# Optimization experiments

Hardware: AMD Instinct MI355X
Metric: run time of the kernel (lower is better)

Reference implementation:

```python
import jax, jax.numpy as jnp
import numpy as np

D_MODEL = 1024
NUM_HEADS = 16
D_HEAD = D_MODEL // NUM_HEADS
BATCH, SEQ, MEM = 2, 1024, 1024
TOT = SEQ + MEM


def setup_inputs() -> dict:
    key = jax.random.key(0)
    ks = jax.random.split(key, 16)
    s = 0.02
    return {
        "x": jax.random.normal(ks[0], (BATCH, SEQ, D_MODEL), jnp.float32),
        "mem": jax.random.normal(ks[1], (BATCH, MEM, D_MODEL), jnp.float32),
        "mask": jnp.zeros((1, 1, SEQ, TOT), jnp.float32),
        "rel_enc": jax.random.normal(ks[2], (TOT, D_MODEL), jnp.float32),
        "Wq": jax.random.normal(ks[3], (D_MODEL, D_MODEL), jnp.float32) * s,
        "bq": jnp.zeros((D_MODEL,), jnp.float32),
        "Wke": jax.random.normal(ks[4], (D_MODEL, D_MODEL), jnp.float32) * s,
        "bke": jnp.zeros((D_MODEL,), jnp.float32),
        "Wkr": jax.random.normal(ks[5], (D_MODEL, D_MODEL), jnp.float32) * s,
        "bkr": jnp.zeros((D_MODEL,), jnp.float32),
        "Wv": jax.random.normal(ks[6], (D_MODEL, D_MODEL), jnp.float32) * s,
        "bv": jnp.zeros((D_MODEL,), jnp.float32),
        "Wo": jax.random.normal(ks[7], (D_MODEL, D_MODEL), jnp.float32) * s,
        "bo": jnp.zeros((D_MODEL,), jnp.float32),
    }


def _split_heads(t, b):
    # (b, s, d_model) -> (b, h, s, d_head)
    return t.reshape(b, -1, NUM_HEADS, D_HEAD).transpose(0, 2, 1, 3)


def _rel_enc_shift(arr):
    # arr: (b, h, l, m) -> Transformer-XL shift trick
    b, h, l, m = arr.shape
    arr = jnp.concatenate([arr, jnp.zeros((b, h, l, 1), arr.dtype)], axis=-1)
    arr = arr.reshape(b, h, l * (m + 1))
    return arr[:, :, l - 1:-1].reshape(b, h, l, m)


def reference(x, mem, mask, rel_enc, Wq, bq, Wke, bke, Wkr, bkr, Wv, bv, Wo, bo):
    b, s, _ = x.shape
    x_tilde = jnp.concatenate([mem, x], axis=1)  # (b, tot, d)
    q = _split_heads(x @ Wq + bq, b)             # (b, h, s, dh)
    k = _split_heads(x_tilde @ Wke + bke, b)     # (b, h, tot, dh)
    v = _split_heads(x_tilde @ Wv + bv, b)       # (b, h, tot, dh)
    A = jnp.einsum("bhsd,bhtd->bhst", q, k)      # content scores
    Q = (rel_enc @ Wkr + bkr).reshape(-1, NUM_HEADS, D_HEAD).transpose(1, 0, 2)  # (h, tot, dh)
    B_hat = jnp.einsum("bhsd,htd->bhst", q, Q)
    B = _rel_enc_shift(B_hat)                    # relative-position scores
    scores = (A + B) / jnp.sqrt(jnp.float32(D_HEAD)) + mask * -1e9
    w = jax.nn.softmax(scores, axis=-1)
    out = jnp.einsum("bhst,bhtd->bhsd", w, v)
    out = out.transpose(0, 2, 1, 3).reshape(b, s, D_MODEL)
    return out @ Wo + bo
```

## Files before the change

### kernel.cpp

```cpp
#include <hip/hip_runtime.h>

typedef unsigned short ushort;
typedef unsigned int uint;
typedef __attribute__((ext_vector_type(8))) short short8;
typedef __attribute__((ext_vector_type(4))) float float4v;

#define D_MODEL 1024
#define NH 16
#define DH 64
#define BATCH 2
#define SEQ 1024
#define MEMLEN 1024
#define TOT 2048

__device__ __forceinline__ float b2f(ushort u) {
  return __uint_as_float(((uint)u) << 16);
}
__device__ __forceinline__ ushort f2b(float f) {
  uint i = __float_as_uint(f);
  uint r = (i + 0x7fffu + ((i >> 16) & 1u)) >> 16;
  return (ushort)r;
}
__device__ __forceinline__ void gld16(const ushort* g, ushort* l) {
  __builtin_amdgcn_global_load_lds(
      (const __attribute__((address_space(1))) void*)g,
      (__attribute__((address_space(3))) void*)l, 16, 0, 0);
}

__global__ __launch_bounds__(256) void preproc_kernel(
    const float* __restrict__ x, const float* __restrict__ mem,
    const float* __restrict__ rel, const float* __restrict__ mask,
    ushort* __restrict__ xt, ushort* __restrict__ xb,
    ushort* __restrict__ relb, ushort* __restrict__ maskb) {
  const int bid = blockIdx.x;
  if (bid < 2048) {
    int idx = bid * 256 + threadIdx.x;
    int row = idx >> 7;
    int c8 = (idx & 127) << 3;
    int b = row >> 11;
    int i = row & 2047;
    const float* src = (i < MEMLEN) ? &mem[((b << 10) + i) * D_MODEL]
                                    : &x[((b << 10) + (i - MEMLEN)) * D_MODEL];
    float4 f0 = *(const float4*)(&src[c8]);
    float4 f1 = *(const float4*)(&src[c8 + 4]);
    ushort u[8] = {f2b(f0.x), f2b(f0.y), f2b(f0.z), f2b(f0.w),
                   f2b(f1.x), f2b(f1.y), f2b(f1.z), f2b(f1.w)};
    *(uint4*)(&xt[row * D_MODEL + c8]) = *(const uint4*)u;
    if (i >= MEMLEN)
      *(uint4*)(&xb[((b << 10) + (i - MEMLEN)) * D_MODEL + c8]) =
          *(const uint4*)u;
  } else if (bid < 3072) {
    int idx = (bid - 2048) * 256 + threadIdx.x;
    int base = idx << 3;
    float4 f0 = *(const float4*)(&rel[base]);
    float4 f1 = *(const float4*)(&rel[base + 4]);
    ushort u[8] = {f2b(f0.x), f2b(f0.y), f2b(f0.z), f2b(f0.w),
                   f2b(f1.x), f2b(f1.y), f2b(f1.z), f2b(f1.w)};
    *(uint4*)(&relb[base]) = *(const uint4*)u;
  } else {
    int idx = (bid - 3072) * 256 + threadIdx.x;
    int base = idx << 3;
    float4 f0 = *(const float4*)(&mask[base]);
    float4 f1 = *(const float4*)(&mask[base + 4]);
    ushort u[8] = {f2b(f0.x * -1e9f), f2b(f0.y * -1e9f), f2b(f0.z * -1e9f),
                   f2b(f0.w * -1e9f), f2b(f1.x * -1e9f), f2b(f1.y * -1e9f),
                   f2b(f1.z * -1e9f), f2b(f1.w * -1e9f)};
    *(uint4*)(&maskb[base]) = *(const uint4*)u;
  }
}

__global__ __launch_bounds__(256) void transpose_cvt5_kernel(
    const float* __restrict__ W0, const float* __restrict__ W1,
    const float* __restrict__ W2, const float* __restrict__ W3,
    const float* __restrict__ W4, ushort* __restrict__ T0,
    ushort* __restrict__ T1, ushort* __restrict__ T2, ushort* __restrict__ T3,
    ushort* __restrict__ T4) {
  __shared__ ushort tle[32][33];
  const float* W;
  ushort* T;
  switch (blockIdx.z) {
    case 0: W = W0; T = T0; break;
    case 1: W = W1; T = T1; break;
    case 2: W = W2; T = T2; break;
    case 3: W = W3; T = T3; break;
    default: W = W4; T = T4; break;
  }
  const int bx = blockIdx.x * 32, by = blockIdx.y * 32;
  const int tx = threadIdx.x & 31, ty = threadIdx.x >> 5;
#pragma unroll
  for (int j = 0; j < 32; j += 8)
    tle[ty + j][tx] = f2b(W[(by + ty + j) * 1024 + bx + tx]);
  __syncthreads();
#pragma unroll
  for (int j = 0; j < 32; j += 8)
    T[(bx + ty + j) * 1024 + by + tx] = tle[tx][ty + j];
}

__global__ __launch_bounds__(256) void gemm_fused_kernel(
    const ushort* __restrict__ xt, const ushort* __restrict__ xbrel,
    const ushort* __restrict__ WkeT, const ushort* __restrict__ WqT,
    const ushort* __restrict__ WkrT, const float* __restrict__ bke,
    const float* __restrict__ bv, const float* __restrict__ bq,
    const float* __restrict__ bkr, ushort* __restrict__ kv,
    ushort* __restrict__ qr) {
  __shared__ ushort As[128 * 32];
  __shared__ ushort Bs[128 * 32];
  const int bid = blockIdx.x;
  const bool seg0 = (bid < 512);
  const ushort* A;
  const ushort* BT;
  int m0, n0;
  if (seg0) {
    m0 = (bid & 31) * 128;
    n0 = (bid >> 5) * 128;
    A = xt;
    BT = WkeT;
  } else {
    int g = bid - 512;
    m0 = (g & 31) * 128;
    n0 = (g >> 5) * 128;
    A = xbrel;
    BT = (m0 < 2048) ? WqT : WkrT;
  }
  const int tid = threadIdx.x;
  const int w = tid >> 6, lane = tid & 63, m15 = lane & 15, q4 = lane >> 4;
  const int wm = w & 1, wn = w >> 1;
  float4v acc[4][4] = {};
  const int c0 = tid, c1 = tid + 256;
  const int r0 = c0 >> 2, u0 = (c0 & 3) * 8;
  const int r1 = c1 >> 2, u1 = (c1 & 3) * 8;

  for (int kk = 0; kk < 1024; kk += 32) {
    __syncthreads();
    gld16(&A[(m0 + r0) * 1024 + kk + u0], &As[c0 * 8]);
    gld16(&A[(m0 + r1) * 1024 + kk + u1], &As[c1 * 8]);
    gld16(&BT[(n0 + r0) * 1024 + kk + u0], &Bs[c0 * 8]);
    gld16(&BT[(n0 + r1) * 1024 + kk + u1], &Bs[c1 * 8]);
    __syncthreads();
    short8 af[4], bf[4];
#pragma unroll
    for (int i = 0; i < 4; ++i)
      af[i] = *(const short8*)(&As[(wm * 64 + i * 16 + m15) * 32 + q4 * 8]);
#pragma unroll
    for (int j = 0; j < 4; ++j)
      bf[j] = *(const short8*)(&Bs[(wn * 64 + j * 16 + m15) * 32 + q4 * 8]);
#pragma unroll
    for (int i = 0; i < 4; ++i)
#pragma unroll
      for (int j = 0; j < 4; ++j)
        acc[i][j] =
            __builtin_amdgcn_mfma_f32_16x16x32_bf16(af[i], bf[j], acc[i][j], 0, 0, 0);
  }
#pragma unroll
  for (int j = 0; j < 4; ++j) {
    int col = n0 + wn * 64 + j * 16 + m15;
    if (seg0) {
      if (col < 1024) {
        float bb = bke[col];
#pragma unroll
        for (int i = 0; i < 4; ++i) {
          int rowb = m0 + wm * 64 + i * 16 + q4 * 4;
#pragma unroll
          for (int r = 0; r < 4; ++r)
            kv[(rowb + r) * 2048 + col] = f2b((acc[i][j][r] + bb) * 0.125f);
        }
      } else {
        float bb = bv[col - 1024];
#pragma unroll
        for (int i = 0; i < 4; ++i) {
          int rowb = m0 + wm * 64 + i * 16 + q4 * 4;
          int dg = ((rowb >> 11) << 10) + (col - 1024);
          size_t prow = (size_t)(dg * 2 + ((rowb >> 10) & 1)) * 2048 + 1024 +
                        (rowb & 1023);
          uint lo = (uint)f2b(acc[i][j][0] + bb) |
                    ((uint)f2b(acc[i][j][1] + bb) << 16);
          uint hi = (uint)f2b(acc[i][j][2] + bb) |
                    ((uint)f2b(acc[i][j][3] + bb) << 16);
          *(uint2*)(&kv[prow]) = make_uint2(lo, hi);
        }
      }
    } else {
      float bb = (m0 < 2048) ? bq[col] : bkr[col];
      float sc = (m0 < 2048) ? 1.0f : 0.125f;
#pragma unroll
      for (int i = 0; i < 4; ++i) {
        int rowb = m0 + wm * 64 + i * 16 + q4 * 4;
#pragma unroll
        for (int r = 0; r < 4; ++r)
          qr[(rowb + r) * 1024 + col] = f2b((acc[i][j][r] + bb) * sc);
      }
    }
  }
}

template <int EPI>
__global__ __launch_bounds__(256) void gemm64_kernel(
    const ushort* __restrict__ A, const ushort* __restrict__ BT,
    const float* __restrict__ bias, void* __restrict__ Cout, int M, int N,
    int K) {
  __shared__ ushort As[64 * 32];
  __shared__ ushort Bs[128 * 32];
  const int m0 = blockIdx.x * 64, n0 = blockIdx.y * 128;
  const int tid = threadIdx.x;
  const int w = tid >> 6, lane = tid & 63, m15 = lane & 15, q4 = lane >> 4;
  float4v acc[4][2] = {};
  const int ra = tid >> 2, ua = (tid & 3) * 8;
  const int c0 = tid, c1 = tid + 256;
  const int rb0 = c0 >> 2, ub0 = (c0 & 3) * 8;
  const int rb1 = c1 >> 2, ub1 = (c1 & 3) * 8;

  for (int kk = 0; kk < K; kk += 32) {
    __syncthreads();
    gld16(&A[(m0 + ra) * K + kk + ua], &As[tid * 8]);
    gld16(&BT[(n0 + rb0) * K + kk + ub0], &Bs[c0 * 8]);
    gld16(&BT[(n0 + rb1) * K + kk + ub1], &Bs[c1 * 8]);
    __syncthreads();
    short8 bf[2];
#pragma unroll
    for (int j = 0; j < 2; ++j)
      bf[j] = *(const short8*)(&Bs[(w * 32 + j * 16 + m15) * 32 + q4 * 8]);
#pragma unroll
    for (int i = 0; i < 4; ++i) {
      short8 af = *(const short8*)(&As[(i * 16 + m15) * 32 + q4 * 8]);
#pragma unroll
      for (int j = 0; j < 2; ++j)
        acc[i][j] =
            __builtin_amdgcn_mfma_f32_16x16x32_bf16(af, bf[j], acc[i][j], 0, 0, 0);
    }
  }
#pragma unroll
  for (int j = 0; j < 2; ++j) {
    int col = n0 + w * 32 + j * 16 + m15;
    float bv = bias[col];
#pragma unroll
    for (int i = 0; i < 4; ++i) {
      int rowb = m0 + i * 16 + q4 * 4;
#pragma unroll
      for (int r = 0; r < 4; ++r) {
        float v = acc[i][j][r] + bv;
        if (EPI == 1)
          ((float*)Cout)[(rowb + r) * N + col] = v;
        else
          ((ushort*)Cout)[(rowb + r) * N + col] = f2b(v);
      }
    }
  }
}

__global__ __launch_bounds__(256) void bhat_kernel(
    const ushort* __restrict__ q, const ushort* __restrict__ Qrb,
    const ushort* __restrict__ maskb, ushort* __restrict__ Bh) {
  __shared__ ushort As[2 * 128 * 32];
  __shared__ ushort Bs[2 * 128 * 32];
  const int bs0 = blockIdx.x * 128, u0 = blockIdx.y * 128, h = blockIdx.z;
  const int tid = threadIdx.x;
  const int w = tid >> 6, lane = tid & 63, m15 = lane & 15, q4 = lane >> 4;
  const int wm = w & 1, wn = w >> 1;

#pragma unroll
  for (int c = 0; c < 4; ++c) {
    int unit = c * 256 + tid;
    int row = (unit >> 2) & 127, kh = unit >> 9, cu = unit & 3;
    gld16(&q[(bs0 + row) * 1024 + (h << 6) + kh * 32 + cu * 8], &As[unit * 8]);
    gld16(&Qrb[(u0 + row) * 1024 + (h << 6) + kh * 32 + cu * 8], &Bs[unit * 8]);
  }
  __syncthreads();

  float4v acc[4][4] = {};
#pragma unroll
  for (int kh = 0; kh < 2; ++kh) {
    short8 af[4], bf[4];
#pragma unroll
    for (int i = 0; i < 4; ++i)
      af[i] = *(const short8*)(&As[kh * 4096 + (wm * 64 + i * 16 + m15) * 32 + q4 * 8]);
#pragma unroll
    for (int j = 0; j < 4; ++j)
      bf[j] = *(const short8*)(&Bs[kh * 4096 + (wn * 64 + j * 16 + m15) * 32 + q4 * 8]);
#pragma unroll
    for (int i = 0; i < 4; ++i)
#pragma unroll
      for (int j = 0; j < 4; ++j)
        acc[i][j] =
            __builtin_amdgcn_mfma_f32_16x16x32_bf16(af[i], bf[j], acc[i][j], 0, 0, 0);
  }
  const int b = bs0 >> 10;
  const int s0loc = bs0 & 1023;
  const int outrow0 = ((b << 4) + h) * 1024 + s0loc;
#pragma unroll
  for (int j = 0; j < 4; ++j) {
    int u = u0 + wn * 64 + j * 16 + m15;
#pragma unroll
    for (int i = 0; i < 4; ++i) {
      int rowb = outrow0 + wm * 64 + i * 16 + q4 * 4;
      int spb = s0loc + wm * 64 + i * 16 + q4 * 4;
#pragma unroll
      for (int r = 0; r < 4; ++r) {
        int sp = spb + r;
        bool selA = (u >= 1023 - sp);
        int mrow = selA ? sp : (sp > 0 ? sp - 1 : 0);
        int mcol = selA ? (u + sp - 1023) : (u + sp + 1025);
        float mval = b2f(maskb[mrow * 2048 + mcol]);
        Bh[(rowb + r) * 2048 + u] = f2b(acc[i][j][r] + mval);
      }
    }
  }
}

__global__ __launch_bounds__(256, 2) void attn_kernel(
    const ushort* __restrict__ qb, const ushort* __restrict__ kv,
    const ushort* __restrict__ Bh, const ushort* __restrict__ maskb,
    ushort* __restrict__ attn) {
  __shared__ ushort Pp[4][16 * 36];
  __shared__ float comb[2][16][68];
  __shared__ float csum[32];

  const int tid = threadIdx.x;
  const int w = tid >> 6, lane = tid & 63, m15 = lane & 15, q4 = lane >> 4;
  const int st = w & 1, th = w >> 1;
  const int s0w = blockIdx.x * 32 + st * 16;
  const int h = blockIdx.y, b = blockIdx.z;
  const int s_l = q4 * 4;

  const ushort* qp = &qb[((b << 10) + s0w + m15) * 1024 + (h << 6) + q4 * 8];
  const short8 af0 = *(const short8*)qp;
  const short8 af1 = *(const short8*)(qp + 32);

  const ushort* kvb = &kv[((size_t)(b << 11) * 2048) + (h << 6)];
  const ushort* vrowb =
      &kv[((size_t)(((b << 10) + (h << 6)) << 1) + th) * 2048 + 1024];
  const int bhbase = ((b << 4) + h) << 21;
  ushort* pw = &Pp[w][0];

  int offA[4], offB[4], diagT[4];
  float dm[4];
#pragma unroll
  for (int i = 0; i < 4; ++i) {
    int s = s0w + s_l + i;
    offA[i] = bhbase + (s << 11) - s + 1023;
    offB[i] = bhbase + ((s + 1) << 11) - s - 1026;
    diagT[i] = s + 1025;
    dm[i] = (diagT[i] <= 2047) ? b2f(maskb[s * 2048 + diagT[i]]) : 0.f;
  }

  float lsum4[4] = {0.f, 0.f, 0.f, 0.f};
  float4v oacc[4] = {};
  const int tb = th * 1024;

  auto ldKV = [&](int c, short8 (&K)[2][2], short8 (&V)[4]) {
    const int t0 = tb + c * 32;
#pragma unroll
    for (int nt = 0; nt < 2; ++nt) {
      const ushort* kp = &kvb[(size_t)(t0 + nt * 16 + m15) * 2048 + q4 * 8];
      K[nt][0] = *(const short8*)kp;
      K[nt][1] = *(const short8*)(kp + 32);
    }
    const int tc = c * 32 + q4 * 8;
#pragma unroll
    for (int nd = 0; nd < 4; ++nd)
      V[nd] = *(const short8*)(&vrowb[(size_t)(nd * 16 + m15) * 4096 + tc]);
  };
  auto ldB = [&](int c, ushort (&B)[8]) {
    const int t0 = tb + c * 32;
#pragma unroll
    for (int nt = 0; nt < 2; ++nt)
#pragma unroll
      for (int i = 0; i < 4; ++i) {
        int t = t0 + nt * 16 + m15;
        int off = (t < diagT[i]) ? offA[i] : offB[i];
        B[nt * 4 + i] = Bh[off + t];
      }
  };

  auto chunk = [&](int c, short8 (&K)[2][2], short8 (&V)[4],
                   short8 (&Kp)[2][2], short8 (&Vp)[4], ushort (&Bs)[8]) {
    ushort cur[8];
#pragma unroll
    for (int j = 0; j < 8; ++j) cur[j] = Bs[j];
    if (c + 2 < 32) ldKV(c + 2, Kp, Vp);
    __builtin_amdgcn_sched_barrier(0x38F);
    if (c + 4 < 32) ldB(c + 4, Bs);
    __builtin_amdgcn_sched_barrier(0x38F);
    float4v a0 = {}, a1 = {};
    a0 = __builtin_amdgcn_mfma_f32_16x16x32_bf16(af0, K[0][0], a0, 0, 0, 0);
    a0 = __builtin_amdgcn_mfma_f32_16x16x32_bf16(af1, K[0][1], a0, 0, 0, 0);
    a1 = __builtin_amdgcn_mfma_f32_16x16x32_bf16(af0, K[1][0], a1, 0, 0, 0);
    a1 = __builtin_amdgcn_mfma_f32_16x16x32_bf16(af1, K[1][1], a1, 0, 0, 0);
    const int t0 = tb + c * 32;
#pragma unroll
    for (int nt = 0; nt < 2; ++nt)
#pragma unroll
      for (int i = 0; i < 4; ++i) {
        int t = t0 + nt * 16 + m15;
        float bv = (t == diagT[i]) ? dm[i] : b2f(cur[nt * 4 + i]);
        float a = (nt == 0) ? a0[i] : a1[i];
        float p = __expf(a + bv);
        lsum4[i] += p;
        pw[(s_l + i) * 36 + nt * 16 + m15] = f2b(p);
      }
    short8 pfr = *(const short8*)(&pw[m15 * 36 + q4 * 8]);
#pragma unroll
    for (int nd = 0; nd < 4; ++nd)
      oacc[nd] =
          __builtin_amdgcn_mfma_f32_16x16x32_bf16(pfr, V[nd], oacc[nd], 0, 0, 0);
  };

  short8 K0[2][2], V0[4], K1[2][2], V1[4], K2[2][2], V2[4], K3[2][2], V3[4];
  ushort B0[8], B1[8], B2[8], B3[8];
  ldKV(0, K0, V0);
  ldKV(1, K1, V1);
  __builtin_amdgcn_sched_barrier(0x38F);
  ldB(0, B0);
  ldB(1, B1);
  ldB(2, B2);
  ldB(3, B3);
  __builtin_amdgcn_sched_barrier(0x38F);
  for (int j = 0; j < 8; ++j) {
    const int c = j * 4;
    chunk(c, K0, V0, K2, V2, B0);
    chunk(c + 1, K1, V1, K3, V3, B1);
    chunk(c + 2, K2, V2, K0, V0, B2);
    chunk(c + 3, K3, V3, K1, V1, B3);
  }

#pragma unroll
  for (int i = 0; i < 4; ++i) {
    float v = lsum4[i];
    v += __shfl_xor(v, 1, 64);
    v += __shfl_xor(v, 2, 64);
    v += __shfl_xor(v, 4, 64);
    v += __shfl_xor(v, 8, 64);
    lsum4[i] = v;
  }
  if (th == 1) {
#pragma unroll
    for (int nd = 0; nd < 4; ++nd)
#pragma unroll
      for (int i = 0; i < 4; ++i)
        comb[st][s_l + i][nd * 16 + m15] = oacc[nd][i];
    if (m15 == 0)
#pragma unroll
      for (int i = 0; i < 4; ++i) csum[st * 16 + s_l + i] = lsum4[i];
  }
  __syncthreads();
  if (th == 0) {
#pragma unroll
    for (int i = 0; i < 4; ++i) lsum4[i] += csum[st * 16 + s_l + i];
#pragma unroll
    for (int nd = 0; nd < 4; ++nd)
#pragma unroll
      for (int i = 0; i < 4; ++i) {
        float v = oacc[nd][i] + comb[st][s_l + i][nd * 16 + m15];
        attn[((b << 10) + s0w + s_l + i) * 1024 + (h << 6) + nd * 16 + m15] =
            f2b(v / lsum4[i]);
      }
  }
}

extern "C" void kernel_launch(void* const* d_in, const int* in_sizes, int n_in,
                              void* d_out, int out_size, void* d_ws,
                              size_t ws_size, hipStream_t stream) {
  const float* x = (const float*)d_in[0];
  const float* mem = (const float*)d_in[1];
  const float* mask = (const float*)d_in[2];
  const float* rel = (const float*)d_in[3];
  const float* Wq = (const float*)d_in[4];
  const float* bq = (const float*)d_in[5];
  const float* Wke = (const float*)d_in[6];
  const float* bke = (const float*)d_in[7];
  const float* Wkr = (const float*)d_in[8];
  const float* bkr = (const float*)d_in[9];
  const float* Wv = (const float*)d_in[10];
  const float* bv = (const float*)d_in[11];
  const float* Wo = (const float*)d_in[12];
  const float* bo = (const float*)d_in[13];
  float* out = (float*)d_out;

  ushort* ws = (ushort*)d_ws;
  ushort* xt = ws;
  ushort* xbrel = xt + 4096 * 1024;
  ushort* WqT = xbrel + 4096 * 1024;
  ushort* WkeT = WqT + 1024 * 1024;
  ushort* WvT = WkeT + 1024 * 1024;
  ushort* WkrT = WvT + 1024 * 1024;
  ushort* WoT = WkrT + 1024 * 1024;
  ushort* kv = WoT + 1024 * 1024;
  ushort* qr = kv + 4096 * 2048;
  ushort* attn = qr + 4096 * 1024;
  ushort* maskb = attn + 2048 * 1024;
  ushort* Bh = maskb + 1024 * 2048;
  ushort* relb = xbrel + 2048 * 1024;
  ushort* Qrb = qr + 2048 * 1024;

  preproc_kernel<<<4096, 256, 0, stream>>>(x, mem, rel, mask, xt, xbrel, relb,
                                           maskb);
  transpose_cvt5_kernel<<<dim3(32, 32, 5), 256, 0, stream>>>(
      Wq, Wke, Wkr, Wv, Wo, WqT, WkeT, WkrT, WvT, WoT);

  gemm_fused_kernel<<<768, 256, 0, stream>>>(xt, xbrel, WkeT, WqT, WkrT, bke,
                                             bv, bq, bkr, kv, qr);

  bhat_kernel<<<dim3(16, 16, 16), 256, 0, stream>>>(qr, Qrb, maskb, Bh);

  attn_kernel<<<dim3(SEQ / 32, NH, BATCH), 256, 0, stream>>>(qr, kv, Bh, maskb,
                                                             attn);

  gemm64_kernel<1><<<dim3(32, 8), 256, 0, stream>>>(attn, WoT, bo, out, 2048,
                                                    1024, 1024);
}
```

Measured before the change: 366.4 us.

## Stage K/V/B-hat tiles through LDS with async loads in attention kernel

The attention kernel now uses 64 query rows per block, with each wave owning 16 rows and running over all 2048 keys. This replaces the split-key scheme and its cross-wave combine step. K, V and the shifted B-hat rows are brought into swizzled LDS through a 4-slot global_load_lds pipeline, and explicit vmcnt waits and barriers replace per-thread scattered register loads. The B-hat buffer gets a padded, row-skewed layout (BROW=2056) so that the shifted reads become 16-byte aligned vectors, with a dual-buffer fallback for tiles that straddle the diagonal. In exchange the block count is halved, per-block LDS use grows, and the new indexing adds correctness risk.

```diff
diff --git a/kernel.cpp b/kernel.cpp
--- a/kernel.cpp
+++ b/kernel.cpp
@@ -12,6 +12,8 @@
 #define SEQ 1024
 #define MEMLEN 1024
 #define TOT 2048
+#define BROW 2056
+#define PLN (1024 * BROW)
 
 __device__ __forceinline__ float b2f(ushort u) {
   return __uint_as_float(((uint)u) << 16);
@@ -285,13 +287,12 @@
   }
   const int b = bs0 >> 10;
   const int s0loc = bs0 & 1023;
-  const int outrow0 = ((b << 4) + h) * 1024 + s0loc;
+  const int pbase = ((b << 4) + h) * PLN;
 #pragma unroll
   for (int j = 0; j < 4; ++j) {
     int u = u0 + wn * 64 + j * 16 + m15;
 #pragma unroll
     for (int i = 0; i < 4; ++i) {
-      int rowb = outrow0 + wm * 64 + i * 16 + q4 * 4;
       int spb = s0loc + wm * 64 + i * 16 + q4 * 4;
 #pragma unroll
       for (int r = 0; r < 4; ++r) {
@@ -300,127 +301,160 @@
         int mrow = selA ? sp : (sp > 0 ? sp - 1 : 0);
         int mcol = selA ? (u + sp - 1023) : (u + sp + 1025);
         float mval = b2f(maskb[mrow * 2048 + mcol]);
-        Bh[(rowb + r) * 2048 + u] = f2b(acc[i][j][r] + mval);
+        Bh[pbase + sp * BROW + ((sp + 1) & 7) + u] = f2b(acc[i][j][r] + mval);
       }
     }
   }
 }
 
-__global__ __launch_bounds__(256, 2) void attn_kernel(
+__global__ __launch_bounds__(256) void attn_kernel(
     const ushort* __restrict__ qb, const ushort* __restrict__ kv,
     const ushort* __restrict__ Bh, const ushort* __restrict__ maskb,
     ushort* __restrict__ attn) {
+  __shared__ ushort Ks[4][32 * 64];
+  __shared__ ushort Vs[4][64 * 32];
+  __shared__ ushort BA[4][64 * 32];
+  __shared__ ushort BB[4][64 * 32];
   __shared__ ushort Pp[4][16 * 36];
-  __shared__ float comb[2][16][68];
-  __shared__ float csum[32];
 
   const int tid = threadIdx.x;
   const int w = tid >> 6, lane = tid & 63, m15 = lane & 15, q4 = lane >> 4;
-  const int st = w & 1, th = w >> 1;
-  const int s0w = blockIdx.x * 32 + st * 16;
+  const int s0 = blockIdx.x * 64;
   const int h = blockIdx.y, b = blockIdx.z;
   const int s_l = q4 * 4;
-
-  const ushort* qp = &qb[((b << 10) + s0w + m15) * 1024 + (h << 6) + q4 * 8];
+  const int sw0 = s0 + w * 16;
+
+  const ushort* qp = &qb[((b << 10) + sw0 + m15) * 1024 + (h << 6) + q4 * 8];
   const short8 af0 = *(const short8*)qp;
   const short8 af1 = *(const short8*)(qp + 32);
 
   const ushort* kvb = &kv[((size_t)(b << 11) * 2048) + (h << 6)];
-  const ushort* vrowb =
-      &kv[((size_t)(((b << 10) + (h << 6)) << 1) + th) * 2048 + 1024];
-  const int bhbase = ((b << 4) + h) << 21;
+  const size_t vbase = ((size_t)((b << 10) + (h << 6)) * 2) * 2048;
+  const int pbase = ((b << 4) + h) * PLN;
   ushort* pw = &Pp[w][0];
 
-  int offA[4], offB[4], diagT[4];
   float dm[4];
+  int diagT[4];
 #pragma unroll
   for (int i = 0; i < 4; ++i) {
-    int s = s0w + s_l + i;
-    offA[i] = bhbase + (s << 11) - s + 1023;
-    offB[i] = bhbase + ((s + 1) << 11) - s - 1026;
+    int s = sw0 + s_l + i;
     diagT[i] = s + 1025;
     dm[i] = (diagT[i] <= 2047) ? b2f(maskb[s * 2048 + diagT[i]]) : 0.f;
   }
+  asm volatile("s_waitcnt vmcnt(0)" ::: "memory");
+  __builtin_amdgcn_sched_barrier(0);
+
+  const int rK = tid >> 3, cK = tid & 7;
+  const int rV = tid >> 2, cV = tid & 3;
+  const int rB = tid >> 2, cB = tid & 3;
+  const int sB = s0 + rB;
+  const int offA_l = pbase + sB * BROW + ((sB + 1) & 7) - sB + 1023;
+  const int offB_l = pbase + (sB + 1) * BROW + ((sB + 2) & 7) - sB - 1026;
+  const int segK = cK ^ (rK & 7);
+  const int segV = cV ^ ((rV >> 2) & 3);
+  const int segB = cB ^ ((rB >> 2) & 3);
 
   float lsum4[4] = {0.f, 0.f, 0.f, 0.f};
   float4v oacc[4] = {};
-  const int tb = th * 1024;
-
-  auto ldKV = [&](int c, short8 (&K)[2][2], short8 (&V)[4]) {
-    const int t0 = tb + c * 32;
-#pragma unroll
-    for (int nt = 0; nt < 2; ++nt) {
-      const ushort* kp = &kvb[(size_t)(t0 + nt * 16 + m15) * 2048 + q4 * 8];
-      K[nt][0] = *(const short8*)kp;
-      K[nt][1] = *(const short8*)(kp + 32);
+
+#define STAGE(c, sl)                                                          \
+  {                                                                           \
+    const int t0_ = (c) * 32;                                                 \
+    gld16(&kvb[(size_t)(t0_ + rK) * 2048 + segK * 8], &Ks[sl][tid * 8]);      \
+    gld16(&kv[vbase + ((size_t)rV * 2 + (t0_ >> 10)) * 2048 + 1024 +          \
+              (t0_ & 1023) + segV * 8],                                       \
+          &Vs[sl][tid * 8]);                                                  \
+    int t8_ = t0_ + segB * 8;                                                 \
+    int offa_ = (t8_ <= sB + 1025) ? offA_l : offB_l;                         \
+    gld16(&Bh[offa_ + t8_], &BA[sl][tid * 8]);                                \
+    bool str_ = (t0_ + 31 >= s0 + 1018) && (t0_ <= s0 + 1088);                \
+    int offb_ = str_ ? offB_l : offa_;                                        \
+    gld16(&Bh[offb_ + t8_], &BB[sl][tid * 8]);                                \
+  }
+
+#define WAITV(n)                                                              \
+  __builtin_amdgcn_sched_barrier(0);                                          \
+  asm volatile("s_waitcnt vmcnt(" #n ")" ::: "memory");                       \
+  __builtin_amdgcn_sched_barrier(0);                                          \
+  __builtin_amdgcn_s_barrier();
+
+  auto compute = [&](int c, int sl) {
+    const int t0 = c * 32;
+    short8 Kf[2][2];
+#pragma unroll
+    for (int nt = 0; nt < 2; ++nt)
+#pragma unroll
+      for (int ko = 0; ko < 2; ++ko)
+        Kf[nt][ko] = *(const short8*)(&Ks[sl][(nt * 16 + m15) * 64 +
+                                              (((q4 + 4 * ko) ^ (m15 & 7)) << 3)]);
+    short8 Vf[4];
+#pragma unroll
+    for (int nd = 0; nd < 4; ++nd) {
+      int d = nd * 16 + m15;
+      Vf[nd] = *(const short8*)(&Vs[sl][d * 32 + ((q4 ^ ((d >> 2) & 3)) << 3)]);
     }
-    const int tc = c * 32 + q4 * 8;
-#pragma unroll
-    for (int nd = 0; nd < 4; ++nd)
-      V[nd] = *(const short8*)(&vrowb[(size_t)(nd * 16 + m15) * 4096 + tc]);
-  };
-  auto ldB = [&](int c, ushort (&B)[8]) {
-    const int t0 = tb + c * 32;
-#pragma unroll
-    for (int nt = 0; nt < 2; ++nt)
-#pragma unroll
-      for (int i = 0; i < 4; ++i) {
-        int t = t0 + nt * 16 + m15;
-        int off = (t < diagT[i]) ? offA[i] : offB[i];
-        B[nt * 4 + i] = Bh[off + t];
-      }
-  };
-
-  auto chunk = [&](int c, short8 (&K)[2][2], short8 (&V)[4],
-                   short8 (&Kp)[2][2], short8 (&Vp)[4], ushort (&Bs)[8]) {
-    ushort cur[8];
-#pragma unroll
-    for (int j = 0; j < 8; ++j) cur[j] = Bs[j];
-    if (c + 2 < 32) ldKV(c + 2, Kp, Vp);
-    __builtin_amdgcn_sched_barrier(0x38F);
-    if (c + 4 < 32) ldB(c + 4, Bs);
-    __builtin_amdgcn_sched_barrier(0x38F);
     float4v a0 = {}, a1 = {};
-    a0 = __builtin_amdgcn_mfma_f32_16x16x32_bf16(af0, K[0][0], a0, 0, 0, 0);
-    a0 = __builtin_amdgcn_mfma_f32_16x16x32_bf16(af1, K[0][1], a0, 0, 0, 0);
-    a1 = __builtin_amdgcn_mfma_f32_16x16x32_bf16(af0, K[1][0], a1, 0, 0, 0);
-    a1 = __builtin_amdgcn_mfma_f32_16x16x32_bf16(af1, K[1][1], a1, 0, 0, 0);
-    const int t0 = tb + c * 32;
-#pragma unroll
-    for (int nt = 0; nt < 2; ++nt)
-#pragma unroll
-      for (int i = 0; i < 4; ++i) {
-        int t = t0 + nt * 16 + m15;
-        float bv = (t == diagT[i]) ? dm[i] : b2f(cur[nt * 4 + i]);
-        float a = (nt == 0) ? a0[i] : a1[i];
-        float p = __expf(a + bv);
-        lsum4[i] += p;
-        pw[(s_l + i) * 36 + nt * 16 + m15] = f2b(p);
-      }
+    a0 = __builtin_amdgcn_mfma_f32_16x16x32_bf16(af0, Kf[0][0], a0, 0, 0, 0);
+    a0 = __builtin_amdgcn_mfma_f32_16x16x32_bf16(af1, Kf[0][1], a0, 0, 0, 0);
+    a1 = __builtin_amdgcn_mfma_f32_16x16x32_bf16(af0, Kf[1][0], a1, 0, 0, 0);
+    a1 = __builtin_amdgcn_mfma_f32_16x16x32_bf16(af1, Kf[1][1], a1, 0, 0, 0);
+    const bool strad = (t0 + 31 >= s0 + 1018) && (t0 <= s0 + 1088);
+    if (!strad) {
+#pragma unroll
+      for (int nt = 0; nt < 2; ++nt)
+#pragma unroll
+        for (int i = 0; i < 4; ++i) {
+          int rr = (w << 4) + s_l + i;
+          int cc = nt * 16 + m15;
+          ushort bu = BA[sl][rr * 32 + (((cc >> 3) ^ q4) << 3) + (cc & 7)];
+          float a = nt ? a1[i] : a0[i];
+          float p = __expf(a + b2f(bu));
+          lsum4[i] += p;
+          pw[(s_l + i) * 36 + cc] = f2b(p);
+        }
+    } else {
+#pragma unroll
+      for (int nt = 0; nt < 2; ++nt)
+#pragma unroll
+        for (int i = 0; i < 4; ++i) {
+          int rr = (w << 4) + s_l + i;
+          int cc = nt * 16 + m15;
+          int t = t0 + cc;
+          int li = rr * 32 + (((cc >> 3) ^ q4) << 3) + (cc & 7);
+          int s = sw0 + s_l + i;
+          float va = b2f(BA[sl][li]);
+          float vb = b2f(BB[sl][li]);
+          int t8 = t & ~7;
+          float bval = (t == diagT[i])
+                           ? dm[i]
+                           : ((t > diagT[i] && t8 <= s + 1025) ? vb : va);
+          float a = nt ? a1[i] : a0[i];
+          float p = __expf(a + bval);
+          lsum4[i] += p;
+          pw[(s_l + i) * 36 + cc] = f2b(p);
+        }
+    }
     short8 pfr = *(const short8*)(&pw[m15 * 36 + q4 * 8]);
 #pragma unroll
     for (int nd = 0; nd < 4; ++nd)
       oacc[nd] =
-          __builtin_amdgcn_mfma_f32_16x16x32_bf16(pfr, V[nd], oacc[nd], 0, 0, 0);
+          __builtin_amdgcn_mfma_f32_16x16x32_bf16(pfr, Vf[nd], oacc[nd], 0, 0, 0);
   };
 
-  short8 K0[2][2], V0[4], K1[2][2], V1[4], K2[2][2], V2[4], K3[2][2], V3[4];
-  ushort B0[8], B1[8], B2[8], B3[8];
-  ldKV(0, K0, V0);
-  ldKV(1, K1, V1);
-  __builtin_amdgcn_sched_barrier(0x38F);
-  ldB(0, B0);
-  ldB(1, B1);
-  ldB(2, B2);
-  ldB(3, B3);
-  __builtin_amdgcn_sched_barrier(0x38F);
-  for (int j = 0; j < 8; ++j) {
+  STAGE(0, 0);
+  STAGE(1, 1);
+  STAGE(2, 2);
+  for (int j = 0; j < 15; ++j) {
     const int c = j * 4;
-    chunk(c, K0, V0, K2, V2, B0);
-    chunk(c + 1, K1, V1, K3, V3, B1);
-    chunk(c + 2, K2, V2, K0, V0, B2);
-    chunk(c + 3, K3, V3, K1, V1, B3);
-  }
+    STAGE(c + 3, 3); WAITV(12); compute(c, 0); __builtin_amdgcn_s_barrier();
+    STAGE(c + 4, 0); WAITV(12); compute(c + 1, 1); __builtin_amdgcn_s_barrier();
+    STAGE(c + 5, 1); WAITV(12); compute(c + 2, 2); __builtin_amdgcn_s_barrier();
+    STAGE(c + 6, 2); WAITV(12); compute(c + 3, 3); __builtin_amdgcn_s_barrier();
+  }
+  STAGE(63, 3); WAITV(12); compute(60, 0); __builtin_amdgcn_s_barrier();
+  WAITV(8);  compute(61, 1); __builtin_amdgcn_s_barrier();
+  WAITV(4);  compute(62, 2); __builtin_amdgcn_s_barrier();
+  WAITV(0);  compute(63, 3);
 
 #pragma unroll
   for (int i = 0; i < 4; ++i) {
@@ -431,29 +465,14 @@
     v += __shfl_xor(v, 8, 64);
     lsum4[i] = v;
   }
-  if (th == 1) {
-#pragma unroll
-    for (int nd = 0; nd < 4; ++nd)
-#pragma unroll
-      for (int i = 0; i < 4; ++i)
-        comb[st][s_l + i][nd * 16 + m15] = oacc[nd][i];
-    if (m15 == 0)
-#pragma unroll
-      for (int i = 0; i < 4; ++i) csum[st * 16 + s_l + i] = lsum4[i];
-  }
-  __syncthreads();
-  if (th == 0) {
-#pragma unroll
-    for (int i = 0; i < 4; ++i) lsum4[i] += csum[st * 16 + s_l + i];
-#pragma unroll
-    for (int nd = 0; nd < 4; ++nd)
-#pragma unroll
-      for (int i = 0; i < 4; ++i) {
-        float v = oacc[nd][i] + comb[st][s_l + i][nd * 16 + m15];
-        attn[((b << 10) + s0w + s_l + i) * 1024 + (h << 6) + nd * 16 + m15] =
-            f2b(v / lsum4[i]);
-      }
-  }
+#pragma unroll
+  for (int nd = 0; nd < 4; ++nd)
+#pragma unroll
+    for (int i = 0; i < 4; ++i)
+      attn[((b << 10) + sw0 + s_l + i) * 1024 + (h << 6) + nd * 16 + m15] =
+          f2b(oacc[nd][i] / lsum4[i]);
+#undef STAGE
+#undef WAITV
 }
 
 extern "C" void kernel_launch(void* const* d_in, const int* in_sizes, int n_in,
@@ -501,8 +520,8 @@
 
   bhat_kernel<<<dim3(16, 16, 16), 256, 0, stream>>>(qr, Qrb, maskb, Bh);
 
-  attn_kernel<<<dim3(SEQ / 32, NH, BATCH), 256, 0, stream>>>(qr, kv, Bh, maskb,
-                                                             attn);
+  attn_kernel<<<dim3(16, NH, BATCH), 256, 0, stream>>>(qr, kv, Bh, maskb,
+                                                       attn);
 
   gemm64_kernel<1><<<dim3(32, 8), 256, 0, stream>>>(attn, WoT, bo, out, 2048,
                                                     1024, 1024);
```

Result: faster. 314.1 us (-14.3%).
